# Performance work log

Measured on AMD Instinct MI355X. Metric: run time of the kernel, lower is better.

Reference implementation:

```python
import jax, jax.numpy as jnp
import numpy as np

N, F_NODE, DIM, H, K, OUT, L = 200000, 16, 3, 128, 20, 4, 4


def setup_inputs() -> dict:
    key = jax.random.key(0)
    ks = jax.random.split(key, 10)
    x = jax.random.normal(ks[0], (N, F_NODE), jnp.float32)
    pos = jax.random.normal(ks[1], (N, DIM), jnp.float32)
    y = jax.random.normal(ks[2], (DIM,), jnp.float32)
    # eigenvector-like basis, roughly orthonormal columns scale
    phi = jax.random.normal(ks[3], (N, K), jnp.float32) / np.sqrt(N).astype(np.float32)
    # torch Linear convention: W is [out, in], y = x @ W.T + b
    lift_w = jax.random.normal(ks[4], (H, F_NODE + 2 * DIM), jnp.float32) * 0.05
    lift_b = jnp.zeros((H,), jnp.float32)
    lin_w = jax.random.normal(ks[5], (L, H, H), jnp.float32) * 0.05  # per-layer, bias=False
    kernel = jax.random.normal(ks[6], (L, K, H, H), jnp.float32) * 0.05
    lower_w = jax.random.normal(ks[7], (OUT, H), jnp.float32) * 0.05
    lower_b = jnp.zeros((OUT,), jnp.float32)
    return dict(x=x, pos=pos, y=y, phi=phi, lift_w=lift_w, lift_b=lift_b,
                lin_w=lin_w, kernel=kernel, lower_w=lower_w, lower_b=lower_b)


def reference(x, pos, y, phi, lift_w, lift_b, lin_w, kernel, lower_w, lower_b):
    # lift: concat node feats, positions, broadcast global y -> [N, F_NODE+2*DIM]
    h = jnp.concatenate([x, pos, y * jnp.ones_like(pos)], axis=1) @ lift_w.T + lift_b
    # pinv(phi) is identical every layer in the original; compute once. [K, N]
    phi_pinv = jnp.linalg.pinv(phi)
    for l in range(L):
        v = phi_pinv @ h                              # [K, H] spectral coefficients
        rv = jnp.einsum('kij,kj->ki', kernel[l], v)   # batched mode matvec (= nested vmap)
        h = jax.nn.elu(h @ lin_w[l].T + phi @ rv)     # [N, H]
    return h @ lower_w.T + lower_b                    # [N, OUT]
```

## Files before the change

### kernel.cpp

```cpp
#include <hip/hip_runtime.h>
#include <math.h>

#define Nn 200000
#define NT 3125

typedef __attribute__((ext_vector_type(8))) short short8;
typedef __attribute__((ext_vector_type(16))) float floatx16;

#define SWZ4(row, g) (((g) ^ ((row) & 7)) << 2)

__device__ __forceinline__ unsigned rnbf(float x) {
    unsigned u = __builtin_bit_cast(unsigned, x);
    return (u + 0x7fffu + ((u >> 16) & 1u)) >> 16;
}
__device__ __forceinline__ float asf(unsigned u) { return __builtin_bit_cast(float, u); }
__device__ __forceinline__ unsigned packf(float x) {
    unsigned hb = rnbf(x);
    float fh = asf(hb << 16);
    unsigned lb = rnbf(x - fh);
    return hb | (lb << 16);
}
__device__ __forceinline__ float unpackf(unsigned p) {
    return asf(p << 16) + asf(p & 0xffff0000u);
}
__device__ __forceinline__ void permsplit(const unsigned* e, short8& hi, short8& lo) {
    uint4 h, l;
    h.x = __builtin_amdgcn_perm(e[1], e[0], 0x05040100u);
    h.y = __builtin_amdgcn_perm(e[3], e[2], 0x05040100u);
    h.z = __builtin_amdgcn_perm(e[5], e[4], 0x05040100u);
    h.w = __builtin_amdgcn_perm(e[7], e[6], 0x05040100u);
    l.x = __builtin_amdgcn_perm(e[1], e[0], 0x07060302u);
    l.y = __builtin_amdgcn_perm(e[3], e[2], 0x07060302u);
    l.z = __builtin_amdgcn_perm(e[5], e[4], 0x07060302u);
    l.w = __builtin_amdgcn_perm(e[7], e[6], 0x07060302u);
    hi = __builtin_bit_cast(short8, h);
    lo = __builtin_bit_cast(short8, l);
}
__device__ __forceinline__ void permsplit2(uint4 q0, uint4 q1, short8& hi, short8& lo) {
    unsigned e[8] = { q0.x, q0.y, q0.z, q0.w, q1.x, q1.y, q1.z, q1.w };
    permsplit(e, hi, lo);
}

__device__ __forceinline__ void pt_accum(const unsigned* As, const unsigned* Ph,
                                         float* __restrict__ PTc_blk, int t) {
    int lane = t & 63, w = t >> 6;
    int ln = lane & 31, hw = lane >> 5;
    int j0 = w * 32;
    floatx16 ap;
#pragma unroll
    for (int i = 0; i < 16; i++) ap[i] = 0.f;
#pragma unroll
    for (int ks = 0; ks < 4; ks++) {
        unsigned pa[8], e[8];
#pragma unroll
        for (int j = 0; j < 8; j++) {
            int node = ks * 16 + 8 * hw + j;
            pa[j] = Ph[node * 32 + SWZ4(node, ln >> 2) + (ln & 3)];
            int col = j0 + ln;
            e[j] = As[node * 128 + SWZ4(node, col >> 2) + (col & 3)];
        }
        short8 a_hi, a_lo, b_hi, b_lo;
        permsplit(pa, a_hi, a_lo);
        permsplit(e, b_hi, b_lo);
        ap = __builtin_amdgcn_mfma_f32_32x32x16_bf16(a_hi, b_hi, ap, 0, 0, 0);
        ap = __builtin_amdgcn_mfma_f32_32x32x16_bf16(a_lo, b_hi, ap, 0, 0, 0);
        ap = __builtin_amdgcn_mfma_f32_32x32x16_bf16(a_hi, b_lo, ap, 0, 0, 0);
    }
#pragma unroll
    for (int r = 0; r < 16; r++) {
        int mode = (r & 3) + 8 * (r >> 2) + 4 * hw;
        if (mode < 20) unsafeAtomicAdd(&PTc_blk[mode * 128 + j0 + ln], ap[r]);
    }
}

__global__ void ptreduce_k(const float* __restrict__ PTc, float* __restrict__ PT) {
    int j = blockIdx.x * 128 + threadIdx.x;
    float s0 = 0.f, s1 = 0.f, s2 = 0.f, s3 = 0.f;
#pragma unroll
    for (int c = 0; c < 64; c += 4) {
        s0 += PTc[(size_t)c * 2560 + j];
        s1 += PTc[(size_t)(c + 1) * 2560 + j];
        s2 += PTc[(size_t)(c + 2) * 2560 + j];
        s3 += PTc[(size_t)(c + 3) * 2560 + j];
    }
    PT[j] = (s0 + s1) + (s2 + s3);
}

__global__ void bias_fold_k(const float* __restrict__ y, const float* __restrict__ lw,
                            const float* __restrict__ lb, float* __restrict__ b2) {
    int j = threadIdx.x;
    float s = lb[j];
#pragma unroll
    for (int d = 0; d < 3; d++) s += y[d] * lw[j * 22 + 19 + d];
    b2[j] = s;
}

__global__ void wsplit_k(const float* __restrict__ lw, unsigned short* __restrict__ Wh,
                         unsigned short* __restrict__ Wl) {
    int i = blockIdx.x * 256 + threadIdx.x;
    float w = lw[i];
    unsigned hb = rnbf(w);
    float fh = asf(hb << 16);
    unsigned lb = rnbf(w - fh);
    Wh[i] = (unsigned short)hb;
    Wl[i] = (unsigned short)lb;
}

__global__ __launch_bounds__(256) void lift_k(const float* __restrict__ x,
                                              const float* __restrict__ pos,
                                              const float* __restrict__ phi,
                                              const float* __restrict__ lw,
                                              const float* __restrict__ b2,
                                              unsigned* __restrict__ hpk,
                                              float* __restrict__ PTc) {
    __shared__ union {
        struct { float xs[64][21]; float Wc[20][132]; } a;
        unsigned As[64 * 128];
    } sm;
    __shared__ unsigned Ph[64 * 32];
    int t = threadIdx.x;
    int n0 = blockIdx.x * 64;
    {
        int n = t >> 2, f4 = (t & 3) * 4;
        float4 xv = *(const float4*)(x + (size_t)(n0 + n) * 16 + f4);
        sm.a.xs[n][f4 + 0] = xv.x; sm.a.xs[n][f4 + 1] = xv.y;
        sm.a.xs[n][f4 + 2] = xv.z; sm.a.xs[n][f4 + 3] = xv.w;
    }
    if (t < 192) { int n = t / 3, d = t % 3; sm.a.xs[n][16 + d] = pos[(size_t)(n0 + n) * 3 + d]; }
    if (t < 64) sm.a.xs[t][19] = 1.f;
    for (int idx = t; idx < 2560; idx += 256) {
        int k = idx >> 7, j = idx & 127;
        sm.a.Wc[k][j] = (k < 19) ? lw[j * 22 + k] : b2[j];
    }
    for (int idx = t; idx < 2048; idx += 256) {
        int row = idx >> 5, kk = idx & 31;
        float pv = (kk < 20) ? phi[(size_t)(n0 + row) * 20 + kk] : 0.f;
        Ph[row * 32 + SWZ4(row, kk >> 2) + (kk & 3)] = packf(pv);
    }
    __syncthreads();
    int tx = t & 31, ty = t >> 5, i0 = tx * 4;
    float acc[8][4];
#pragma unroll
    for (int m = 0; m < 8; m++)
#pragma unroll
        for (int c = 0; c < 4; c++) acc[m][c] = 0.f;
#pragma unroll 4
    for (int k = 0; k < 20; k++) {
        float4 w = *(const float4*)&sm.a.Wc[k][i0];
#pragma unroll
        for (int m = 0; m < 8; m++) {
            float a = sm.a.xs[ty + 8 * m][k];
            acc[m][0] += a * w.x; acc[m][1] += a * w.y;
            acc[m][2] += a * w.z; acc[m][3] += a * w.w;
        }
    }
    __syncthreads();
#pragma unroll
    for (int m = 0; m < 8; m++) {
        uint4 o;
        o.x = packf(acc[m][0]); o.y = packf(acc[m][1]);
        o.z = packf(acc[m][2]); o.w = packf(acc[m][3]);
        int row = ty + 8 * m;
        *(uint4*)&hpk[(size_t)(n0 + row) * 128 + i0] = o;
        *(uint4*)&sm.As[row * 128 + SWZ4(row, tx)] = o;
    }
    __syncthreads();
    pt_accum(sm.As, Ph, PTc + (size_t)(blockIdx.x & 63) * 2560, t);
}

__global__ void gram_k(const float* __restrict__ phi, float* __restrict__ G) {
    __shared__ float ph[64 * 20];
    int t = threadIdx.x;
    int i0 = t / 20, j0 = t % 20;
    int p1 = t + 256;
    int i1 = p1 / 20, j1 = p1 % 20;
    float a0 = 0.f, a1 = 0.f;
    for (int tile = blockIdx.x; tile < NT; tile += gridDim.x) {
        const float* src = phi + tile * 1280;
        for (int idx = t; idx < 1280; idx += 256) ph[idx] = src[idx];
        __syncthreads();
        for (int n = 0; n < 64; n++) {
            const float* r = ph + n * 20;
            a0 += r[i0] * r[j0];
            if (p1 < 400) a1 += r[i1] * r[j1];
        }
        __syncthreads();
    }
    unsafeAtomicAdd(&G[t], a0);
    if (p1 < 400) unsafeAtomicAdd(&G[p1], a1);
}

__global__ void ginv_k(const float* __restrict__ G, float* __restrict__ Gi) {
    __shared__ float A[20][40];
    __shared__ float colp[20];
    __shared__ float piv;
    int t = threadIdx.x;
    for (int idx = t; idx < 400; idx += 64) {
        int r = idx / 20, c = idx % 20;
        A[r][c] = G[idx];
        A[r][c + 20] = (r == c) ? 1.f : 0.f;
    }
    __syncthreads();
    for (int p = 0; p < 20; p++) {
        if (t == 0) piv = 1.f / A[p][p];
        __syncthreads();
        for (int c = t; c < 40; c += 64) A[p][c] *= piv;
        __syncthreads();
        if (t < 20) colp[t] = A[t][p];
        __syncthreads();
        for (int e = t; e < 800; e += 64) {
            int r = e / 40, c = e % 40;
            if (r != p) A[r][c] -= colp[r] * A[p][c];
        }
        __syncthreads();
    }
    for (int idx = t; idx < 400; idx += 64) {
        int r = idx / 20, c = idx % 20;
        Gi[idx] = A[r][c + 20];
    }
}

__global__ void rv_k(const float* __restrict__ Gi, const float* __restrict__ PT,
                     const float* __restrict__ kern_l,
                     unsigned short* __restrict__ RVh, unsigned short* __restrict__ RVl) {
    __shared__ __align__(16) float v[128];
    __shared__ float part[128];
    int k = blockIdx.x;
    int t = threadIdx.x;
    if (t < 128) {
        const float* gr = Gi + k * 20;
        float s = 0.f;
#pragma unroll
        for (int m = 0; m < 20; m++) s += gr[m] * PT[m * 128 + t];
        v[t] = s;
    }
    __syncthreads();
    int i = t & 127, half = t >> 7;
    const float* kr = kern_l + (size_t)(k * 128 + i) * 128 + half * 64;
    const float* vk = v + half * 64;
    float acc = 0.f;
#pragma unroll 4
    for (int jj = 0; jj < 64; jj += 4) {
        float4 kv = *(const float4*)(kr + jj);
        float4 vv = *(const float4*)(vk + jj);
        acc += kv.x * vv.x + kv.y * vv.y + kv.z * vv.z + kv.w * vv.w;
    }
    if (half) part[i] = acc;
    __syncthreads();
    if (!half) {
        float rv = acc + part[i];
        unsigned hb = rnbf(rv);
        float fh = asf(hb << 16);
        unsigned lb = rnbf(rv - fh);
        RVh[i * 32 + k] = (unsigned short)hb;
        RVl[i * 32 + k] = (unsigned short)lb;
    }
}

__global__ __launch_bounds__(256, 3) void update_k(unsigned* __restrict__ hpk,
                                                   const float* __restrict__ phi,
                                                   const unsigned short* __restrict__ Wh,
                                                   const unsigned short* __restrict__ Wl,
                                                   const unsigned short* __restrict__ RVh,
                                                   const unsigned short* __restrict__ RVl,
                                                   float* __restrict__ ptn,
                                                   const float* __restrict__ low_w,
                                                   const float* __restrict__ low_b,
                                                   float* __restrict__ outp) {
    __shared__ __align__(16) unsigned As[64 * 128];
    __shared__ __align__(16) unsigned Ph[64 * 32];
    int t = threadIdx.x;
    int n0 = blockIdx.x * 64;
    for (int idx = t; idx < 2048; idx += 256) {
        int row = idx >> 5, g = idx & 31;
        uint4 v = *(const uint4*)(hpk + (size_t)(n0 + row) * 128 + g * 4);
        *(uint4*)&As[row * 128 + SWZ4(row, g)] = v;
    }
    for (int idx = t; idx < 2048; idx += 256) {
        int row = idx >> 5, kk = idx & 31;
        float pv = (kk < 20) ? phi[(size_t)(n0 + row) * 20 + kk] : 0.f;
        Ph[row * 32 + SWZ4(row, kk >> 2) + (kk & 3)] = packf(pv);
    }
    __syncthreads();

    int lane = t & 63, w = t >> 6;
    int ln = lane & 31, hw = lane >> 5;
    int r0 = (w >> 1) * 32, ct0 = (w & 1) * 64;
    int arow = r0 + ln;

    floatx16 acc0, acc1;
#pragma unroll
    for (int i = 0; i < 16; i++) { acc0[i] = 0.f; acc1[i] = 0.f; }

    const unsigned short* whp0 = Wh + (size_t)(ct0 + ln) * 128 + 8 * hw;
    const unsigned short* wlp0 = Wl + (size_t)(ct0 + ln) * 128 + 8 * hw;
    const unsigned short* whp1 = whp0 + 32 * 128;
    const unsigned short* wlp1 = wlp0 + 32 * 128;
    const unsigned* abase = As + arow * 128;

    uint4 wh0c = *(const uint4*)(whp0), wl0c = *(const uint4*)(wlp0);
    uint4 wh1c = *(const uint4*)(whp1), wl1c = *(const uint4*)(wlp1);
    uint4 aq0c = *(const uint4*)(abase + SWZ4(arow, 2 * hw));
    uint4 aq1c = *(const uint4*)(abase + SWZ4(arow, 2 * hw + 1));
#pragma unroll
    for (int ks = 0; ks < 8; ks++) {
        uint4 wh0n, wl0n, wh1n, wl1n, aq0n, aq1n;
        if (ks < 7) {
            int k1 = (ks + 1) * 16;
            int ga = 4 * (ks + 1) + 2 * hw;
            wh0n = *(const uint4*)(whp0 + k1); wl0n = *(const uint4*)(wlp0 + k1);
            wh1n = *(const uint4*)(whp1 + k1); wl1n = *(const uint4*)(wlp1 + k1);
            aq0n = *(const uint4*)(abase + SWZ4(arow, ga));
            aq1n = *(const uint4*)(abase + SWZ4(arow, ga + 1));
        }
        short8 a_hi, a_lo;
        permsplit2(aq0c, aq1c, a_hi, a_lo);
        short8 b0h = __builtin_bit_cast(short8, wh0c);
        short8 b0l = __builtin_bit_cast(short8, wl0c);
        short8 b1h = __builtin_bit_cast(short8, wh1c);
        short8 b1l = __builtin_bit_cast(short8, wl1c);
        acc0 = __builtin_amdgcn_mfma_f32_32x32x16_bf16(a_hi, b0h, acc0, 0, 0, 0);
        acc0 = __builtin_amdgcn_mfma_f32_32x32x16_bf16(a_lo, b0h, acc0, 0, 0, 0);
        acc0 = __builtin_amdgcn_mfma_f32_32x32x16_bf16(a_hi, b0l, acc0, 0, 0, 0);
        acc1 = __builtin_amdgcn_mfma_f32_32x32x16_bf16(a_hi, b1h, acc1, 0, 0, 0);
        acc1 = __builtin_amdgcn_mfma_f32_32x32x16_bf16(a_lo, b1h, acc1, 0, 0, 0);
        acc1 = __builtin_amdgcn_mfma_f32_32x32x16_bf16(a_hi, b1l, acc1, 0, 0, 0);
        if (ks < 7) {
            wh0c = wh0n; wl0c = wl0n; wh1c = wh1n; wl1c = wl1n;
            aq0c = aq0n; aq1c = aq1n;
        }
    }

    const unsigned* pbase = Ph + arow * 32;
#pragma unroll
    for (int ks = 0; ks < 2; ks++) {
        int k0 = ks * 16;
        int gr = 4 * ks + 2 * hw;
        uint4 q0 = *(const uint4*)(pbase + SWZ4(arow, gr));
        uint4 q1 = *(const uint4*)(pbase + SWZ4(arow, gr + 1));
        short8 a_hi, a_lo;
        permsplit2(q0, q1, a_hi, a_lo);
        short8 b0h = __builtin_bit_cast(short8, *(const uint4*)(RVh + (size_t)(ct0 + ln) * 32 + k0 + 8 * hw));
        short8 b0l = __builtin_bit_cast(short8, *(const uint4*)(RVl + (size_t)(ct0 + ln) * 32 + k0 + 8 * hw));
        short8 b1h = __builtin_bit_cast(short8, *(const uint4*)(RVh + (size_t)(ct0 + 32 + ln) * 32 + k0 + 8 * hw));
        short8 b1l = __builtin_bit_cast(short8, *(const uint4*)(RVl + (size_t)(ct0 + 32 + ln) * 32 + k0 + 8 * hw));
        acc0 = __builtin_amdgcn_mfma_f32_32x32x16_bf16(a_hi, b0h, acc0, 0, 0, 0);
        acc0 = __builtin_amdgcn_mfma_f32_32x32x16_bf16(a_lo, b0h, acc0, 0, 0, 0);
        acc0 = __builtin_amdgcn_mfma_f32_32x32x16_bf16(a_hi, b0l, acc0, 0, 0, 0);
        acc1 = __builtin_amdgcn_mfma_f32_32x32x16_bf16(a_hi, b1h, acc1, 0, 0, 0);
        acc1 = __builtin_amdgcn_mfma_f32_32x32x16_bf16(a_lo, b1h, acc1, 0, 0, 0);
        acc1 = __builtin_amdgcn_mfma_f32_32x32x16_bf16(a_hi, b1l, acc1, 0, 0, 0);
    }

    unsigned p0[16], p1[16];
#pragma unroll
    for (int r = 0; r < 16; r++) {
        float v0 = acc0[r];
        v0 = v0 > 0.f ? v0 : __expf(v0) - 1.f;
        p0[r] = packf(v0);
        float v1 = acc1[r];
        v1 = v1 > 0.f ? v1 : __expf(v1) - 1.f;
        p1[r] = packf(v1);
    }
    if (!outp) {
#pragma unroll
        for (int r = 0; r < 16; r++) {
            int row = (r & 3) + 8 * (r >> 2) + 4 * hw;
            size_t base = (size_t)(n0 + r0 + row) * 128;
            hpk[base + ct0 + ln] = p0[r];
            hpk[base + ct0 + 32 + ln] = p1[r];
        }
    }
    if (ptn || outp) {
        __syncthreads();
#pragma unroll
        for (int r = 0; r < 16; r++) {
            int row = r0 + (r & 3) + 8 * (r >> 2) + 4 * hw;
            int c0 = ct0 + ln, c1 = ct0 + 32 + ln;
            As[row * 128 + SWZ4(row, c0 >> 2) + (c0 & 3)] = p0[r];
            As[row * 128 + SWZ4(row, c1 >> 2) + (c1 & 3)] = p1[r];
        }
        __syncthreads();
        if (outp) {
            int n = t >> 2, o = t & 3;
            float s = low_b[o];
            const float* lwo = low_w + o * 128;
#pragma unroll 8
            for (int g = 0; g < 32; g++) {
                uint4 q = *(const uint4*)&As[n * 128 + SWZ4(n, g)];
                float4 lv = *(const float4*)(lwo + g * 4);
                s += unpackf(q.x) * lv.x + unpackf(q.y) * lv.y +
                     unpackf(q.z) * lv.z + unpackf(q.w) * lv.w;
            }
            outp[(size_t)(n0 + n) * 4 + o] = s;
        } else {
            pt_accum(As, Ph, ptn + (size_t)(blockIdx.x & 63) * 2560, t);
        }
    }
}

extern "C" void kernel_launch(void* const* d_in, const int* in_sizes, int n_in,
                              void* d_out, int out_size, void* d_ws, size_t ws_size,
                              hipStream_t stream) {
    (void)in_sizes; (void)n_in; (void)out_size; (void)ws_size;
    const float* x       = (const float*)d_in[0];
    const float* pos     = (const float*)d_in[1];
    const float* y       = (const float*)d_in[2];
    const float* phi     = (const float*)d_in[3];
    const float* lift_w  = (const float*)d_in[4];
    const float* lift_b  = (const float*)d_in[5];
    const float* lin_w   = (const float*)d_in[6];
    const float* kern    = (const float*)d_in[7];
    const float* lower_w = (const float*)d_in[8];
    const float* lower_b = (const float*)d_in[9];
    float* out = (float*)d_out;

    char* ws = (char*)d_ws;
    unsigned* hpk = (unsigned*)ws;
    size_t off = (size_t)Nn * 128 * 4;
    float* b2  = (float*)(ws + off);       off += 512;
    float* G   = (float*)(ws + off);       off += 1600;
    float* Gi  = (float*)(ws + off);       off += 1600;
    off = (off + 15) & ~(size_t)15;
    float* PT  = (float*)(ws + off);       off += 10240;
    float* PTc = (float*)(ws + off);       off += 64 * 2560 * 4;
    unsigned short* W_hi = (unsigned short*)(ws + off);  off += 131072;
    unsigned short* W_lo = (unsigned short*)(ws + off);  off += 131072;
    unsigned short* RVh  = (unsigned short*)(ws + off);  off += 8192;
    unsigned short* RVl  = (unsigned short*)(ws + off);  off += 8192;

    hipMemsetAsync(G, 0, 1600, stream);
    hipMemsetAsync(PTc, 0, 64 * 2560 * 4, stream);
    hipMemsetAsync(RVh, 0, 8192, stream);
    hipMemsetAsync(RVl, 0, 8192, stream);
    bias_fold_k<<<1, 128, 0, stream>>>(y, lift_w, lift_b, b2);
    wsplit_k<<<256, 256, 0, stream>>>(lin_w, W_hi, W_lo);
    lift_k<<<NT, 256, 0, stream>>>(x, pos, phi, lift_w, b2, hpk, PTc);
    gram_k<<<256, 256, 0, stream>>>(phi, G);
    ginv_k<<<1, 64, 0, stream>>>(G, Gi);
    ptreduce_k<<<20, 128, 0, stream>>>(PTc, PT);

    for (int l = 0; l < 4; l++) {
        rv_k<<<20, 256, 0, stream>>>(Gi, PT, kern + (size_t)l * 20 * 128 * 128, RVh, RVl);
        float* ptc = (l < 3) ? PTc : (float*)nullptr;
        if (ptc) hipMemsetAsync(ptc, 0, 64 * 2560 * 4, stream);
        update_k<<<NT, 256, 0, stream>>>(hpk, phi, W_hi + (size_t)l * 16384,
                                         W_lo + (size_t)l * 16384, RVh, RVl, ptc,
                                         lower_w, lower_b,
                                         (l == 3) ? out : (float*)nullptr);
        if (ptc) ptreduce_k<<<20, 128, 0, stream>>>(PTc, PT);
    }
}
```

Before: 659.1 us.

## Compute final lower projection with split-bf16 MFMA and raise update occupancy

Result: faster. 621.3 us (-5.7%).

```diff
diff --git a/kernel.cpp b/kernel.cpp
--- a/kernel.cpp
+++ b/kernel.cpp
@@ -95,15 +95,20 @@
     b2[j] = s;
 }
 
-__global__ void wsplit_k(const float* __restrict__ lw, unsigned short* __restrict__ Wh,
-                         unsigned short* __restrict__ Wl) {
+__global__ void wsplit_k(const float* __restrict__ lw, const float* __restrict__ low_w,
+                         unsigned short* __restrict__ Wh, unsigned short* __restrict__ Wl,
+                         unsigned short* __restrict__ LWh, unsigned short* __restrict__ LWl) {
     int i = blockIdx.x * 256 + threadIdx.x;
-    float w = lw[i];
+    float w;
+    unsigned short *ph, *pl;
+    int idx;
+    if (i < 65536) { w = lw[i]; ph = Wh; pl = Wl; idx = i; }
+    else           { w = low_w[i - 65536]; ph = LWh; pl = LWl; idx = i - 65536; }
     unsigned hb = rnbf(w);
     float fh = asf(hb << 16);
     unsigned lb = rnbf(w - fh);
-    Wh[i] = (unsigned short)hb;
-    Wl[i] = (unsigned short)lb;
+    ph[idx] = (unsigned short)hb;
+    pl[idx] = (unsigned short)lb;
 }
 
 __global__ __launch_bounds__(256) void lift_k(const float* __restrict__ x,
@@ -257,14 +262,15 @@
     }
 }
 
-__global__ __launch_bounds__(256, 3) void update_k(unsigned* __restrict__ hpk,
+__global__ __launch_bounds__(256, 4) void update_k(unsigned* __restrict__ hpk,
                                                    const float* __restrict__ phi,
                                                    const unsigned short* __restrict__ Wh,
                                                    const unsigned short* __restrict__ Wl,
                                                    const unsigned short* __restrict__ RVh,
                                                    const unsigned short* __restrict__ RVl,
                                                    float* __restrict__ ptn,
-                                                   const float* __restrict__ low_w,
+                                                   const unsigned short* __restrict__ LWh,
+                                                   const unsigned short* __restrict__ LWl,
                                                    const float* __restrict__ low_b,
                                                    float* __restrict__ outp) {
     __shared__ __align__(16) unsigned As[64 * 128];
@@ -382,17 +388,46 @@
         }
         __syncthreads();
         if (outp) {
-            int n = t >> 2, o = t & 3;
-            float s = low_b[o];
-            const float* lwo = low_w + o * 128;
-#pragma unroll 8
-            for (int g = 0; g < 32; g++) {
-                uint4 q = *(const uint4*)&As[n * 128 + SWZ4(n, g)];
-                float4 lv = *(const float4*)(lwo + g * 4);
-                s += unpackf(q.x) * lv.x + unpackf(q.y) * lv.y +
-                     unpackf(q.z) * lv.z + unpackf(q.w) * lv.w;
+            float* scr = (float*)Ph;
+            int kh = w & 1;
+            floatx16 ap;
+#pragma unroll
+            for (int i = 0; i < 16; i++) ap[i] = 0.f;
+#pragma unroll
+            for (int kk = 0; kk < 4; kk++) {
+                int ks = kh * 4 + kk;
+                int ga = 4 * ks + 2 * hw;
+                uint4 q0 = *(const uint4*)(abase + SWZ4(arow, ga));
+                uint4 q1 = *(const uint4*)(abase + SWZ4(arow, ga + 1));
+                short8 a_hi, a_lo;
+                permsplit2(q0, q1, a_hi, a_lo);
+                short8 bh = { 0, 0, 0, 0, 0, 0, 0, 0 };
+                short8 bl = { 0, 0, 0, 0, 0, 0, 0, 0 };
+                if (ln < 4) {
+                    bh = __builtin_bit_cast(short8, *(const uint4*)(LWh + ln * 128 + ks * 16 + 8 * hw));
+                    bl = __builtin_bit_cast(short8, *(const uint4*)(LWl + ln * 128 + ks * 16 + 8 * hw));
+                }
+                ap = __builtin_amdgcn_mfma_f32_32x32x16_bf16(a_hi, bh, ap, 0, 0, 0);
+                ap = __builtin_amdgcn_mfma_f32_32x32x16_bf16(a_lo, bh, ap, 0, 0, 0);
+                ap = __builtin_amdgcn_mfma_f32_32x32x16_bf16(a_hi, bl, ap, 0, 0, 0);
             }
-            outp[(size_t)(n0 + n) * 4 + o] = s;
+            if (kh == 1 && ln < 4) {
+#pragma unroll
+                for (int r = 0; r < 16; r++) {
+                    int row = (r & 3) + 8 * (r >> 2) + 4 * hw;
+                    scr[(w >> 1) * 128 + row * 4 + ln] = ap[r];
+                }
+            }
+            __syncthreads();
+            if (kh == 0 && ln < 4) {
+                float b = low_b[ln];
+#pragma unroll
+                for (int r = 0; r < 16; r++) {
+                    int row = (r & 3) + 8 * (r >> 2) + 4 * hw;
+                    float s = ap[r] + scr[(w >> 1) * 128 + row * 4 + ln] + b;
+                    outp[(size_t)(n0 + r0 + row) * 4 + ln] = s;
+                }
+            }
         } else {
             pt_accum(As, Ph, ptn + (size_t)(blockIdx.x & 63) * 2560, t);
         }
@@ -428,13 +463,15 @@
     unsigned short* W_lo = (unsigned short*)(ws + off);  off += 131072;
     unsigned short* RVh  = (unsigned short*)(ws + off);  off += 8192;
     unsigned short* RVl  = (unsigned short*)(ws + off);  off += 8192;
+    unsigned short* LWh  = (unsigned short*)(ws + off);  off += 1024;
+    unsigned short* LWl  = (unsigned short*)(ws + off);  off += 1024;
 
     hipMemsetAsync(G, 0, 1600, stream);
     hipMemsetAsync(PTc, 0, 64 * 2560 * 4, stream);
     hipMemsetAsync(RVh, 0, 8192, stream);
     hipMemsetAsync(RVl, 0, 8192, stream);
     bias_fold_k<<<1, 128, 0, stream>>>(y, lift_w, lift_b, b2);
-    wsplit_k<<<256, 256, 0, stream>>>(lin_w, W_hi, W_lo);
+    wsplit_k<<<258, 256, 0, stream>>>(lin_w, lower_w, W_hi, W_lo, LWh, LWl);
     lift_k<<<NT, 256, 0, stream>>>(x, pos, phi, lift_w, b2, hpk, PTc);
     gram_k<<<256, 256, 0, stream>>>(phi, G);
     ginv_k<<<1, 64, 0, stream>>>(G, Gi);
@@ -446,7 +483,7 @@
         if (ptc) hipMemsetAsync(ptc, 0, 64 * 2560 * 4, stream);
         update_k<<<NT, 256, 0, stream>>>(hpk, phi, W_hi + (size_t)l * 16384,
                                          W_lo + (size_t)l * 16384, RVh, RVl, ptc,
-                                         lower_w, lower_b,
+                                         LWh, LWl, lower_b,
                                          (l == 3) ? out : (float*)nullptr);
         if (ptc) ptreduce_k<<<20, 128, 0, stream>>>(PTc, PT);
     }
```
